# Kernel tuning notes

Measured on AMD Instinct MI355X. Metric: run time of the kernel, lower is better.

Reference implementation:

```python
import jax, jax.numpy as jnp
import numpy as np

F = 64  # filters per ConvLSTM layer

def hard_sigmoid(x):
    return jnp.clip(0.2 * x + 0.5, 0.0, 1.0)

def conv2d_same(x, w):
    # x: (B,H,W,C), w: (kh,kw,Cin,Cout)
    return jax.lax.conv_general_dilated(x, w, window_strides=(1, 1), padding='SAME',
                                        dimension_numbers=('NHWC', 'HWIO', 'NHWC'))

def convlstm2d(x_seq, Wx, Wh, b):
    # x_seq: (B,T,H,W,Cin) -> (B,T,H,W,F). Keras gate order: i, f, c, o.
    B, T, H, W, _ = x_seq.shape
    h0 = jnp.zeros((B, H, W, F), x_seq.dtype)
    c0 = h0
    def step(carry, x_t):
        h, c = carry
        z = conv2d_same(x_t, Wx) + conv2d_same(h, Wh) + b  # (B,H,W,4F)
        i, f, g, o = jnp.split(z, 4, axis=-1)
        c = hard_sigmoid(f) * c + hard_sigmoid(i) * jnp.tanh(g)
        h = hard_sigmoid(o) * jnp.tanh(c)
        return (h, c), h
    xs = jnp.moveaxis(x_seq, 1, 0)  # time-major
    _, hs = jax.lax.scan(step, (h0, c0), xs)
    return jnp.moveaxis(hs, 0, 1)

def setup_inputs() -> dict:
    key = jax.random.key(0)
    ks = jax.random.split(key, 16)
    B, n_steps, n_feat, n_out = 64, 2048, 64, 1
    s = 0.05
    def rn(k, shape):
        return jax.random.normal(k, shape, dtype=jnp.float32) * s
    inp = {'x': jax.random.normal(ks[0], (B, 1, 1, n_steps, n_feat), dtype=jnp.float32)}
    kernels = [(10, n_feat), (5, F), (10, F), (5, F)]
    for li, (kh, cin) in enumerate(kernels, start=1):
        inp[f'W{li}x'] = rn(ks[3 * li - 2], (kh, 1, cin, 4 * F))
        inp[f'W{li}h'] = rn(ks[3 * li - 1], (kh, 1, F, 4 * F))
        inp[f'b{li}'] = jnp.zeros((4 * F,), jnp.float32)
    flat_dim = 1 * 1 * n_steps * F
    inp['D1w'] = rn(ks[13], (flat_dim, 64))
    inp['D1b'] = jnp.zeros((64,), jnp.float32)
    inp['D2w'] = rn(ks[14], (64, n_out))
    inp['D2b'] = jnp.zeros((n_out,), jnp.float32)
    return inp

def reference(x, W1x, W1h, b1, W2x, W2h, b2, W3x, W3h, b3, W4x, W4h, b4, D1w, D1b, D2w, D2b):
    h = convlstm2d(x, W1x, W1h, b1)   # dropout layers are identity at inference
    h = convlstm2d(h, W2x, W2h, b2)
    h = convlstm2d(h, W3x, W3h, b3)
    h = convlstm2d(h, W4x, W4h, b4)
    flat = h.reshape(h.shape[0], -1)  # (B, T*H*W*F)
    y = jax.nn.relu(flat @ D1w + D1b)
    return y @ D2w + D2b
```

## Files before the change

### kernel.cpp

```cpp
#include <hip/hip_runtime.h>


#define POS 131072

typedef __attribute__((ext_vector_type(8))) short bf16x8;
typedef __attribute__((ext_vector_type(4))) float f32x4;

__device__ __forceinline__ unsigned short f2bf_rn(float f) {
    unsigned u = __float_as_uint(f);
    u += 0x7FFF + ((u >> 16) & 1);
    return (unsigned short)(u >> 16);
}
__device__ __forceinline__ float bf2f(unsigned short h) {
    return __uint_as_float(((unsigned)h) << 16);
}
__device__ __forceinline__ float hsig(float x) {
    return fminf(fmaxf(fmaf(x, 0.2f, 0.5f), 0.0f), 1.0f);
}
__device__ __forceinline__ float tanh_e(float x) {
    float t = __expf(2.0f * x);
    return 1.0f - __fdividef(2.0f, t + 1.0f);
}

__global__ __launch_bounds__(256) void prep_w(
    const float* __restrict__ W1, const float* __restrict__ W2,
    const float* __restrict__ W3, const float* __restrict__ W4,
    unsigned short* __restrict__ WT)
{
    const int bid = blockIdx.x;
    const int ll = bid / 3;
    const int g  = bid - ll * 3;
    const float* W = (ll == 0) ? (W1 + 4 * 16384) :
                     (ll == 1) ? (W2 + 2 * 16384) :
                     (ll == 2) ? (W3 + 4 * 16384) : (W4 + 2 * 16384);
    const int gofs = (g == 0) ? 0 : ((g == 1) ? 128 : 192);
    unsigned short* hi = WT + ll * (2 * 192 * 64) + (g * 64) * 64;
    unsigned short* lo = hi + 192 * 64;
    const int n  = threadIdx.x & 63;
    const int c0 = threadIdx.x >> 6;
    #pragma unroll
    for (int cc = 0; cc < 16; cc++) {
        int c = cc * 4 + c0;
        float w = W[c * 256 + gofs + n];
        unsigned short h = f2bf_rn(w);
        hi[n * 64 + c] = h;
        lo[n * 64 + c] = f2bf_rn(w - bf2f(h));
    }
}

__global__ __launch_bounds__(256, 4) void fused_mfma(
    const float* __restrict__ x,
    const unsigned short* __restrict__ WT,
    const float* __restrict__ B1, const float* __restrict__ B2,
    const float* __restrict__ B3, const float* __restrict__ B4,
    unsigned short* __restrict__ h4hi, unsigned short* __restrict__ h4lo)
{
    __shared__ unsigned short Hhi[64][72];
    __shared__ unsigned short Hlo[64][72];

    const int t = threadIdx.x;
    const int lane = t & 63;
    const int w = t >> 6;
    const int tx = lane & 15;
    const int quad = lane >> 4;
    const int n = 16 * w + tx;
    const int pbase = blockIdx.x * 64;

    {
        const float4* xv = (const float4*)(x + (size_t)pbase * 64);
        #pragma unroll
        for (int k = 0; k < 4; k++) {
            int lin4 = t + k * 256;
            int p = lin4 >> 4;
            int c0 = (lin4 & 15) * 4;
            float4 v = xv[lin4];
            const float* vp = (const float*)&v;
            unsigned short h0 = f2bf_rn(vp[0]), h1 = f2bf_rn(vp[1]);
            unsigned short h2 = f2bf_rn(vp[2]), h3 = f2bf_rn(vp[3]);
            unsigned hh01 = (unsigned)h0 | ((unsigned)h1 << 16);
            unsigned hh23 = (unsigned)h2 | ((unsigned)h3 << 16);
            unsigned ll01 = (unsigned)f2bf_rn(vp[0] - bf2f(h0)) |
                            ((unsigned)f2bf_rn(vp[1] - bf2f(h1)) << 16);
            unsigned ll23 = (unsigned)f2bf_rn(vp[2] - bf2f(h2)) |
                            ((unsigned)f2bf_rn(vp[3] - bf2f(h3)) << 16);
            *(uint2*)&Hhi[p][c0] = make_uint2(hh01, hh23);
            *(uint2*)&Hlo[p][c0] = make_uint2(ll01, ll23);
        }
    }
    __syncthreads();

    #pragma unroll 1
    for (int l = 0; l < 4; l++) {
        const unsigned short* wl = WT + l * (2 * 192 * 64);
        const float* Bb = (l == 0) ? B1 : (l == 1) ? B2 : (l == 2) ? B3 : B4;
        const float bi = Bb[n];
        const float bg = Bb[128 + n];
        const float bo = Bb[192 + n];

        f32x4 acc[4][3];
        #pragma unroll
        for (int m = 0; m < 4; m++) {
            acc[m][0] = (f32x4){bi, bi, bi, bi};
            acc[m][1] = (f32x4){bg, bg, bg, bg};
            acc[m][2] = (f32x4){bo, bo, bo, bo};
        }

        #pragma unroll
        for (int ks = 0; ks < 2; ks++) {
            bf16x8 Bh[3], Bl[3];
            #pragma unroll
            for (int g = 0; g < 3; g++) {
                const unsigned short* bp = wl + (g * 64 + n) * 64 + ks * 32 + quad * 8;
                Bh[g] = *(const bf16x8*)bp;
                Bl[g] = *(const bf16x8*)(bp + 192 * 64);
            }
            #pragma unroll
            for (int m = 0; m < 4; m++) {
                bf16x8 Ah = *(const bf16x8*)&Hhi[m * 16 + tx][ks * 32 + quad * 8];
                bf16x8 Al = *(const bf16x8*)&Hlo[m * 16 + tx][ks * 32 + quad * 8];
                #pragma unroll
                for (int g = 0; g < 3; g++) {
                    acc[m][g] = __builtin_amdgcn_mfma_f32_16x16x32_bf16(Ah, Bh[g], acc[m][g], 0, 0, 0);
                    acc[m][g] = __builtin_amdgcn_mfma_f32_16x16x32_bf16(Ah, Bl[g], acc[m][g], 0, 0, 0);
                    acc[m][g] = __builtin_amdgcn_mfma_f32_16x16x32_bf16(Al, Bh[g], acc[m][g], 0, 0, 0);
                }
            }
        }

        __syncthreads();
        #pragma unroll
        for (int m = 0; m < 4; m++) {
            #pragma unroll
            for (int r = 0; r < 4; r++) {
                float cs = hsig(acc[m][0][r]) * tanh_e(acc[m][1][r]);
                float h  = hsig(acc[m][2][r]) * tanh_e(cs);
                int p = m * 16 + quad * 4 + r;
                unsigned short hh = f2bf_rn(h);
                Hhi[p][n] = hh;
                Hlo[p][n] = f2bf_rn(h - bf2f(hh));
            }
        }
        __syncthreads();
    }

    #pragma unroll
    for (int i = 0; i < 2; i++) {
        int lin8 = t + i * 256;
        int p = lin8 >> 3;
        int c0 = (lin8 & 7) * 8;
        uint4 vh = *(const uint4*)&Hhi[p][c0];
        uint4 vl = *(const uint4*)&Hlo[p][c0];
        size_t g = (size_t)(pbase + p) * 64 + c0;
        *(uint4*)(h4hi + g) = vh;
        *(uint4*)(h4lo + g) = vl;
    }
}

__global__ __launch_bounds__(256) void d1_mfma(
    const unsigned short* __restrict__ Ahig, const unsigned short* __restrict__ Alog,
    const float* __restrict__ Bw, float* __restrict__ part)
{
    __shared__ unsigned short Ahi[64][72], Alo[64][72];
    __shared__ unsigned short Bhi[64][66], Blo[64][66];
    const int t = threadIdx.x;
    const int kb = blockIdx.x;
    const int lane = t & 63, w = t >> 6;
    const int tx = lane & 15, quad = lane >> 4;
    const int n = 16 * w + tx;

    #pragma unroll
    for (int i = 0; i < 2; i++) {
        int lin8 = t + i * 256;
        int row = lin8 >> 3;
        int c0 = (lin8 & 7) * 8;
        size_t g = (size_t)row * 131072 + (size_t)kb * 64 + c0;
        *(uint4*)&Ahi[row][c0] = *(const uint4*)(Ahig + g);
        *(uint4*)&Alo[row][c0] = *(const uint4*)(Alog + g);
    }
    #pragma unroll
    for (int i = 0; i < 4; i++) {
        int lin4 = t + i * 256;
        int k = lin4 >> 4;
        int j0 = (lin4 & 15) * 4;
        float4 v = *(const float4*)(Bw + (size_t)(kb * 64 + k) * 64 + j0);
        const float* vp = (const float*)&v;
        unsigned short h0 = f2bf_rn(vp[0]), h1 = f2bf_rn(vp[1]);
        unsigned short h2 = f2bf_rn(vp[2]), h3 = f2bf_rn(vp[3]);
        *(unsigned*)&Bhi[k][j0]     = (unsigned)h0 | ((unsigned)h1 << 16);
        *(unsigned*)&Bhi[k][j0 + 2] = (unsigned)h2 | ((unsigned)h3 << 16);
        *(unsigned*)&Blo[k][j0]     = (unsigned)f2bf_rn(vp[0] - bf2f(h0)) |
                                      ((unsigned)f2bf_rn(vp[1] - bf2f(h1)) << 16);
        *(unsigned*)&Blo[k][j0 + 2] = (unsigned)f2bf_rn(vp[2] - bf2f(h2)) |
                                      ((unsigned)f2bf_rn(vp[3] - bf2f(h3)) << 16);
    }
    __syncthreads();

    f32x4 acc[4];
    #pragma unroll
    for (int m = 0; m < 4; m++) acc[m] = (f32x4){0.0f, 0.0f, 0.0f, 0.0f};

    #pragma unroll
    for (int ks = 0; ks < 2; ks++) {
        bf16x8 Bh, Bl;
        #pragma unroll
        for (int jj = 0; jj < 8; jj++) {
            int k = ks * 32 + quad * 8 + jj;
            Bh[jj] = (short)Bhi[k][n];
            Bl[jj] = (short)Blo[k][n];
        }
        #pragma unroll
        for (int m = 0; m < 4; m++) {
            bf16x8 Ah = *(const bf16x8*)&Ahi[m * 16 + tx][ks * 32 + quad * 8];
            bf16x8 Al = *(const bf16x8*)&Alo[m * 16 + tx][ks * 32 + quad * 8];
            acc[m] = __builtin_amdgcn_mfma_f32_16x16x32_bf16(Ah, Bh, acc[m], 0, 0, 0);
            acc[m] = __builtin_amdgcn_mfma_f32_16x16x32_bf16(Ah, Bl, acc[m], 0, 0, 0);
            acc[m] = __builtin_amdgcn_mfma_f32_16x16x32_bf16(Al, Bh, acc[m], 0, 0, 0);
        }
    }

    float* dst = part + (size_t)kb * 4096;
    #pragma unroll
    for (int m = 0; m < 4; m++)
        #pragma unroll
        for (int r = 0; r < 4; r++)
            dst[(m * 16 + quad * 4 + r) * 64 + n] = acc[m][r];
}

__global__ __launch_bounds__(256) void d1_reduce1(
    const float* __restrict__ part, float* __restrict__ part2)
{
    __shared__ float red[4][64];
    const int b = blockIdx.x >> 3;
    const int g = blockIdx.x & 7;
    const int t = threadIdx.x;
    const int j = t & 63, s = t >> 6;
    float acc = 0.0f;
    #pragma unroll 4
    for (int m = 0; m < 64; m++)
        acc += part[(size_t)(g * 256 + s + 4 * m) * 4096 + b * 64 + j];
    red[s][j] = acc;
    __syncthreads();
    if (t < 64)
        part2[(size_t)(b * 8 + g) * 64 + t] =
            red[0][t] + red[1][t] + red[2][t] + red[3][t];
}

__global__ __launch_bounds__(64) void d1_reduce2(
    const float* __restrict__ part2, const float* __restrict__ D1b,
    const float* __restrict__ D2w, const float* __restrict__ D2b,
    float* __restrict__ out)
{
    const int b = blockIdx.x;
    const int j = threadIdx.x;
    float v = D1b[j];
    #pragma unroll
    for (int g = 0; g < 8; g++) v += part2[(size_t)(b * 8 + g) * 64 + j];
    v = fmaxf(v, 0.0f) * D2w[j];
    #pragma unroll
    for (int off = 32; off > 0; off >>= 1)
        v += __shfl_down(v, off, 64);
    if (j == 0) out[b] = v + D2b[0];
}

extern "C" void kernel_launch(void* const* d_in, const int* in_sizes, int n_in,
                              void* d_out, int out_size, void* d_ws, size_t ws_size,
                              hipStream_t stream) {
    (void)in_sizes; (void)n_in; (void)out_size; (void)ws_size;
    const float* x   = (const float*)d_in[0];
    const float* W1x = (const float*)d_in[1];
    const float* b1  = (const float*)d_in[3];
    const float* W2x = (const float*)d_in[4];
    const float* b2  = (const float*)d_in[6];
    const float* W3x = (const float*)d_in[7];
    const float* b3  = (const float*)d_in[9];
    const float* W4x = (const float*)d_in[10];
    const float* b4  = (const float*)d_in[12];
    const float* D1w = (const float*)d_in[13];
    const float* D1b = (const float*)d_in[14];
    const float* D2w = (const float*)d_in[15];
    const float* D2b = (const float*)d_in[16];
    float* out = (float*)d_out;

    unsigned short* h4hi = (unsigned short*)d_ws;
    unsigned short* h4lo = h4hi + (size_t)POS * 64;
    float* part  = (float*)(h4lo + (size_t)POS * 64);
    float* part2 = part + (size_t)2048 * 4096;
    unsigned short* WT = (unsigned short*)(part2 + 512 * 64);

    prep_w<<<dim3(12), dim3(256), 0, stream>>>(W1x, W2x, W3x, W4x, WT);
    fused_mfma<<<dim3(POS / 64), dim3(256), 0, stream>>>(
        x, WT, b1, b2, b3, b4, h4hi, h4lo);
    d1_mfma<<<dim3(2048), dim3(256), 0, stream>>>(h4hi, h4lo, D1w, part);
    d1_reduce1<<<dim3(512), dim3(256), 0, stream>>>(part, part2);
    d1_reduce2<<<dim3(64), dim3(64), 0, stream>>>(part2, D1b, D2w, D2b, out);
}
```

Before: 213.2 us.

## Prefetch next-layer weights, widen LDS padding, and merge split-K D1 partial reductions

In the fused ConvLSTM kernel, each layer's weight fragments are now held in registers and the next layer's weights are loaded before the gate math, so global loads overlap compute. The gate activations are computed before the barrier rather than after it. The LDS row pitch grows from 72 to 80 elements. The D1 GEMM now runs 4 K-chunks per block, cutting the partial buffer from 2048 to 512 slices, and the two reduction kernels become one 1024-thread kernel, which shrinks partial-sum traffic and drops a launch. The cost is more registers in the fused kernel, which may lower occupancy, and fewer D1 blocks.

Result: faster. 201.6 us (-5.4%).

```diff
diff --git a/kernel.cpp b/kernel.cpp
--- a/kernel.cpp
+++ b/kernel.cpp
@@ -2,6 +2,7 @@
 
 
 #define POS 131072
+#define SH 80
 
 typedef __attribute__((ext_vector_type(8))) short bf16x8;
 typedef __attribute__((ext_vector_type(4))) float f32x4;
@@ -55,8 +56,8 @@
     const float* __restrict__ B3, const float* __restrict__ B4,
     unsigned short* __restrict__ h4hi, unsigned short* __restrict__ h4lo)
 {
-    __shared__ unsigned short Hhi[64][72];
-    __shared__ unsigned short Hlo[64][72];
+    __shared__ unsigned short Hhi[64][SH];
+    __shared__ unsigned short Hlo[64][SH];
 
     const int t = threadIdx.x;
     const int lane = t & 63;
@@ -65,6 +66,21 @@
     const int quad = lane >> 4;
     const int n = 16 * w + tx;
     const int pbase = blockIdx.x * 64;
+
+    bf16x8 Bh[2][3], Bl[2][3];
+    auto loadB = [&](int l) {
+        const unsigned short* wl = WT + l * (2 * 192 * 64);
+        #pragma unroll
+        for (int ks = 0; ks < 2; ks++)
+            #pragma unroll
+            for (int g = 0; g < 3; g++) {
+                const unsigned short* bp = wl + (g * 64 + n) * 64 + ks * 32 + quad * 8;
+                Bh[ks][g] = *(const bf16x8*)bp;
+                Bl[ks][g] = *(const bf16x8*)(bp + 192 * 64);
+            }
+    };
+
+    loadB(0);
 
     {
         const float4* xv = (const float4*)(x + (size_t)pbase * 64);
@@ -91,7 +107,6 @@
 
     #pragma unroll 1
     for (int l = 0; l < 4; l++) {
-        const unsigned short* wl = WT + l * (2 * 192 * 64);
         const float* Bb = (l == 0) ? B1 : (l == 1) ? B2 : (l == 2) ? B3 : B4;
         const float bi = Bb[n];
         const float bg = Bb[128 + n];
@@ -106,40 +121,40 @@
         }
 
         #pragma unroll
-        for (int ks = 0; ks < 2; ks++) {
-            bf16x8 Bh[3], Bl[3];
-            #pragma unroll
-            for (int g = 0; g < 3; g++) {
-                const unsigned short* bp = wl + (g * 64 + n) * 64 + ks * 32 + quad * 8;
-                Bh[g] = *(const bf16x8*)bp;
-                Bl[g] = *(const bf16x8*)(bp + 192 * 64);
-            }
+        for (int ks = 0; ks < 2; ks++)
             #pragma unroll
             for (int m = 0; m < 4; m++) {
                 bf16x8 Ah = *(const bf16x8*)&Hhi[m * 16 + tx][ks * 32 + quad * 8];
                 bf16x8 Al = *(const bf16x8*)&Hlo[m * 16 + tx][ks * 32 + quad * 8];
                 #pragma unroll
                 for (int g = 0; g < 3; g++) {
-                    acc[m][g] = __builtin_amdgcn_mfma_f32_16x16x32_bf16(Ah, Bh[g], acc[m][g], 0, 0, 0);
-                    acc[m][g] = __builtin_amdgcn_mfma_f32_16x16x32_bf16(Ah, Bl[g], acc[m][g], 0, 0, 0);
-                    acc[m][g] = __builtin_amdgcn_mfma_f32_16x16x32_bf16(Al, Bh[g], acc[m][g], 0, 0, 0);
+                    acc[m][g] = __builtin_amdgcn_mfma_f32_16x16x32_bf16(Ah, Bh[ks][g], acc[m][g], 0, 0, 0);
+                    acc[m][g] = __builtin_amdgcn_mfma_f32_16x16x32_bf16(Ah, Bl[ks][g], acc[m][g], 0, 0, 0);
+                    acc[m][g] = __builtin_amdgcn_mfma_f32_16x16x32_bf16(Al, Bh[ks][g], acc[m][g], 0, 0, 0);
                 }
             }
-        }
-
-        __syncthreads();
-        #pragma unroll
-        for (int m = 0; m < 4; m++) {
+
+        if (l < 3) loadB(l + 1);
+
+        float hv[4][4];
+        #pragma unroll
+        for (int m = 0; m < 4; m++)
             #pragma unroll
             for (int r = 0; r < 4; r++) {
                 float cs = hsig(acc[m][0][r]) * tanh_e(acc[m][1][r]);
-                float h  = hsig(acc[m][2][r]) * tanh_e(cs);
+                hv[m][r] = hsig(acc[m][2][r]) * tanh_e(cs);
+            }
+
+        __syncthreads();
+        #pragma unroll
+        for (int m = 0; m < 4; m++)
+            #pragma unroll
+            for (int r = 0; r < 4; r++) {
                 int p = m * 16 + quad * 4 + r;
-                unsigned short hh = f2bf_rn(h);
+                unsigned short hh = f2bf_rn(hv[m][r]);
                 Hhi[p][n] = hh;
-                Hlo[p][n] = f2bf_rn(h - bf2f(hh));
-            }
-        }
+                Hlo[p][n] = f2bf_rn(hv[m][r] - bf2f(hh));
+            }
         __syncthreads();
     }
 
@@ -160,7 +175,7 @@
     const unsigned short* __restrict__ Ahig, const unsigned short* __restrict__ Alog,
     const float* __restrict__ Bw, float* __restrict__ part)
 {
-    __shared__ unsigned short Ahi[64][72], Alo[64][72];
+    __shared__ unsigned short Ahi[64][SH], Alo[64][SH];
     __shared__ unsigned short Bhi[64][66], Blo[64][66];
     const int t = threadIdx.x;
     const int kb = blockIdx.x;
@@ -168,53 +183,58 @@
     const int tx = lane & 15, quad = lane >> 4;
     const int n = 16 * w + tx;
 
-    #pragma unroll
-    for (int i = 0; i < 2; i++) {
-        int lin8 = t + i * 256;
-        int row = lin8 >> 3;
-        int c0 = (lin8 & 7) * 8;
-        size_t g = (size_t)row * 131072 + (size_t)kb * 64 + c0;
-        *(uint4*)&Ahi[row][c0] = *(const uint4*)(Ahig + g);
-        *(uint4*)&Alo[row][c0] = *(const uint4*)(Alog + g);
-    }
-    #pragma unroll
-    for (int i = 0; i < 4; i++) {
-        int lin4 = t + i * 256;
-        int k = lin4 >> 4;
-        int j0 = (lin4 & 15) * 4;
-        float4 v = *(const float4*)(Bw + (size_t)(kb * 64 + k) * 64 + j0);
-        const float* vp = (const float*)&v;
-        unsigned short h0 = f2bf_rn(vp[0]), h1 = f2bf_rn(vp[1]);
-        unsigned short h2 = f2bf_rn(vp[2]), h3 = f2bf_rn(vp[3]);
-        *(unsigned*)&Bhi[k][j0]     = (unsigned)h0 | ((unsigned)h1 << 16);
-        *(unsigned*)&Bhi[k][j0 + 2] = (unsigned)h2 | ((unsigned)h3 << 16);
-        *(unsigned*)&Blo[k][j0]     = (unsigned)f2bf_rn(vp[0] - bf2f(h0)) |
-                                      ((unsigned)f2bf_rn(vp[1] - bf2f(h1)) << 16);
-        *(unsigned*)&Blo[k][j0 + 2] = (unsigned)f2bf_rn(vp[2] - bf2f(h2)) |
-                                      ((unsigned)f2bf_rn(vp[3] - bf2f(h3)) << 16);
-    }
-    __syncthreads();
-
     f32x4 acc[4];
     #pragma unroll
     for (int m = 0; m < 4; m++) acc[m] = (f32x4){0.0f, 0.0f, 0.0f, 0.0f};
 
-    #pragma unroll
-    for (int ks = 0; ks < 2; ks++) {
-        bf16x8 Bh, Bl;
-        #pragma unroll
-        for (int jj = 0; jj < 8; jj++) {
-            int k = ks * 32 + quad * 8 + jj;
-            Bh[jj] = (short)Bhi[k][n];
-            Bl[jj] = (short)Blo[k][n];
-        }
-        #pragma unroll
-        for (int m = 0; m < 4; m++) {
-            bf16x8 Ah = *(const bf16x8*)&Ahi[m * 16 + tx][ks * 32 + quad * 8];
-            bf16x8 Al = *(const bf16x8*)&Alo[m * 16 + tx][ks * 32 + quad * 8];
-            acc[m] = __builtin_amdgcn_mfma_f32_16x16x32_bf16(Ah, Bh, acc[m], 0, 0, 0);
-            acc[m] = __builtin_amdgcn_mfma_f32_16x16x32_bf16(Ah, Bl, acc[m], 0, 0, 0);
-            acc[m] = __builtin_amdgcn_mfma_f32_16x16x32_bf16(Al, Bh, acc[m], 0, 0, 0);
+    #pragma unroll 1
+    for (int sub = 0; sub < 4; sub++) {
+        const int k0 = kb * 256 + sub * 64;
+        if (sub) __syncthreads();
+        #pragma unroll
+        for (int i = 0; i < 2; i++) {
+            int lin8 = t + i * 256;
+            int row = lin8 >> 3;
+            int c0 = (lin8 & 7) * 8;
+            size_t g = (size_t)row * 131072 + k0 + c0;
+            *(uint4*)&Ahi[row][c0] = *(const uint4*)(Ahig + g);
+            *(uint4*)&Alo[row][c0] = *(const uint4*)(Alog + g);
+        }
+        #pragma unroll
+        for (int i = 0; i < 4; i++) {
+            int lin4 = t + i * 256;
+            int k = lin4 >> 4;
+            int j0 = (lin4 & 15) * 4;
+            float4 v = *(const float4*)(Bw + (size_t)(k0 + k) * 64 + j0);
+            const float* vp = (const float*)&v;
+            unsigned short h0 = f2bf_rn(vp[0]), h1 = f2bf_rn(vp[1]);
+            unsigned short h2 = f2bf_rn(vp[2]), h3 = f2bf_rn(vp[3]);
+            *(unsigned*)&Bhi[k][j0]     = (unsigned)h0 | ((unsigned)h1 << 16);
+            *(unsigned*)&Bhi[k][j0 + 2] = (unsigned)h2 | ((unsigned)h3 << 16);
+            *(unsigned*)&Blo[k][j0]     = (unsigned)f2bf_rn(vp[0] - bf2f(h0)) |
+                                          ((unsigned)f2bf_rn(vp[1] - bf2f(h1)) << 16);
+            *(unsigned*)&Blo[k][j0 + 2] = (unsigned)f2bf_rn(vp[2] - bf2f(h2)) |
+                                          ((unsigned)f2bf_rn(vp[3] - bf2f(h3)) << 16);
+        }
+        __syncthreads();
+
+        #pragma unroll
+        for (int ks = 0; ks < 2; ks++) {
+            bf16x8 Bh, Bl;
+            #pragma unroll
+            for (int jj = 0; jj < 8; jj++) {
+                int k = ks * 32 + quad * 8 + jj;
+                Bh[jj] = (short)Bhi[k][n];
+                Bl[jj] = (short)Blo[k][n];
+            }
+            #pragma unroll
+            for (int m = 0; m < 4; m++) {
+                bf16x8 Ah = *(const bf16x8*)&Ahi[m * 16 + tx][ks * 32 + quad * 8];
+                bf16x8 Al = *(const bf16x8*)&Alo[m * 16 + tx][ks * 32 + quad * 8];
+                acc[m] = __builtin_amdgcn_mfma_f32_16x16x32_bf16(Ah, Bh, acc[m], 0, 0, 0);
+                acc[m] = __builtin_amdgcn_mfma_f32_16x16x32_bf16(Ah, Bl, acc[m], 0, 0, 0);
+                acc[m] = __builtin_amdgcn_mfma_f32_16x16x32_bf16(Al, Bh, acc[m], 0, 0, 0);
+            }
         }
     }
 
@@ -226,40 +246,31 @@
             dst[(m * 16 + quad * 4 + r) * 64 + n] = acc[m][r];
 }
 
-__global__ __launch_bounds__(256) void d1_reduce1(
-    const float* __restrict__ part, float* __restrict__ part2)
+__global__ __launch_bounds__(1024) void d1_reduce(
+    const float* __restrict__ part, const float* __restrict__ D1b,
+    const float* __restrict__ D2w, const float* __restrict__ D2b,
+    float* __restrict__ out)
 {
-    __shared__ float red[4][64];
-    const int b = blockIdx.x >> 3;
-    const int g = blockIdx.x & 7;
+    __shared__ float red[16][64];
+    const int b = blockIdx.x;
     const int t = threadIdx.x;
     const int j = t & 63, s = t >> 6;
     float acc = 0.0f;
     #pragma unroll 4
-    for (int m = 0; m < 64; m++)
-        acc += part[(size_t)(g * 256 + s + 4 * m) * 4096 + b * 64 + j];
+    for (int m = 0; m < 32; m++)
+        acc += part[(size_t)(s + 16 * m) * 4096 + b * 64 + j];
     red[s][j] = acc;
     __syncthreads();
-    if (t < 64)
-        part2[(size_t)(b * 8 + g) * 64 + t] =
-            red[0][t] + red[1][t] + red[2][t] + red[3][t];
-}
-
-__global__ __launch_bounds__(64) void d1_reduce2(
-    const float* __restrict__ part2, const float* __restrict__ D1b,
-    const float* __restrict__ D2w, const float* __restrict__ D2b,
-    float* __restrict__ out)
-{
-    const int b = blockIdx.x;
-    const int j = threadIdx.x;
-    float v = D1b[j];
-    #pragma unroll
-    for (int g = 0; g < 8; g++) v += part2[(size_t)(b * 8 + g) * 64 + j];
-    v = fmaxf(v, 0.0f) * D2w[j];
-    #pragma unroll
-    for (int off = 32; off > 0; off >>= 1)
-        v += __shfl_down(v, off, 64);
-    if (j == 0) out[b] = v + D2b[0];
+    if (t < 64) {
+        float v = D1b[t];
+        #pragma unroll
+        for (int s2 = 0; s2 < 16; s2++) v += red[s2][t];
+        v = fmaxf(v, 0.0f) * D2w[t];
+        #pragma unroll
+        for (int off = 32; off > 0; off >>= 1)
+            v += __shfl_down(v, off, 64);
+        if (t == 0) out[b] = v + D2b[0];
+    }
 }
 
 extern "C" void kernel_launch(void* const* d_in, const int* in_sizes, int n_in,
@@ -283,14 +294,12 @@
 
     unsigned short* h4hi = (unsigned short*)d_ws;
     unsigned short* h4lo = h4hi + (size_t)POS * 64;
-    float* part  = (float*)(h4lo + (size_t)POS * 64);
-    float* part2 = part + (size_t)2048 * 4096;
-    unsigned short* WT = (unsigned short*)(part2 + 512 * 64);
+    float* part = (float*)(h4lo + (size_t)POS * 64);
+    unsigned short* WT = (unsigned short*)(part + (size_t)512 * 4096);
 
     prep_w<<<dim3(12), dim3(256), 0, stream>>>(W1x, W2x, W3x, W4x, WT);
     fused_mfma<<<dim3(POS / 64), dim3(256), 0, stream>>>(
         x, WT, b1, b2, b3, b4, h4hi, h4lo);
-    d1_mfma<<<dim3(2048), dim3(256), 0, stream>>>(h4hi, h4lo, D1w, part);
-    d1_reduce1<<<dim3(512), dim3(256), 0, stream>>>(part, part2);
-    d1_reduce2<<<dim3(64), dim3(64), 0, stream>>>(part2, D1b, D2w, D2b, out);
-}
+    d1_mfma<<<dim3(512), dim3(256), 0, stream>>>(h4hi, h4lo, D1w, part);
+    d1_reduce<<<dim3(64), dim3(1024), 0, stream>>>(part, D1b, D2w, D2b, out);
+}
```
